# Optimization experiments

Measured on AMD Instinct MI355X. Metric: run time of the kernel, lower is better.

Reference implementation:

```python
import jax, jax.numpy as jnp
import numpy as np

IN_CHANNELS = 512
NUM_HEADS = 8
HEAD_CH = IN_CHANNELS // NUM_HEADS


def setup_inputs() -> dict:
    key = jax.random.key(0)
    k0, k1, k2, k3, k4 = jax.random.split(key, 5)
    B, C, H, W = 4, IN_CHANNELS, 128, 128
    x = jax.random.normal(k0, (B, C, H, W), dtype=jnp.float32)
    # 1x1 Conv2d weights == per-pixel linear layers over channels
    s_in = 1.0 / np.sqrt(C)
    Wqkv = jax.random.uniform(k1, (3 * C, C), dtype=jnp.float32, minval=-s_in, maxval=s_in)
    bqkv = jax.random.uniform(k2, (3 * C,), dtype=jnp.float32, minval=-s_in, maxval=s_in)
    Wout = jax.random.uniform(k3, (C, C), dtype=jnp.float32, minval=-s_in, maxval=s_in)
    bout = jax.random.uniform(k4, (C,), dtype=jnp.float32, minval=-s_in, maxval=s_in)
    return {"x": x, "Wqkv": Wqkv, "bqkv": bqkv, "Wout": Wout, "bout": bout}


def _axial_attention(x, Wqkv, bqkv, Wout, bout):
    B, C, H, W = x.shape
    nh, d = NUM_HEADS, HEAD_CH
    scale = 1.0 / jnp.sqrt(jnp.asarray(d, dtype=x.dtype))

    # 1x1 conv qkv projection: [B, 3C, H, W]
    qkv = jnp.einsum('bchw,oc->bohw', x, Wqkv) + bqkv[None, :, None, None]
    q, k, v = jnp.split(qkv, 3, axis=1)
    # [B, nh, d, H, W]
    q = q.reshape(B, nh, d, H, W)
    k = k.reshape(B, nh, d, H, W)
    v = v.reshape(B, nh, d, H, W)

    # Row attention: for each row h, attend across width (w over u)
    scores_row = jnp.einsum('bndhw,bndhu->bnhwu', q, k) * scale  # [B,nh,H,W,W]
    probs_row = jax.nn.softmax(scores_row, axis=-1)
    out_row = jnp.einsum('bnhwu,bndhu->bndhw', probs_row, v)  # [B,nh,d,H,W]

    # Column attention: for each column w, attend across height (h over g)
    scores_col = jnp.einsum('bndhw,bndgw->bnwhg', q, k) * scale  # [B,nh,W,H,H]
    probs_col = jax.nn.softmax(scores_col, axis=-1)
    out_col = jnp.einsum('bnwhg,bndgw->bndhw', probs_col, v)  # [B,nh,d,H,W]

    out = (out_row + out_col).reshape(B, C, H, W)
    # 1x1 conv output projection
    return jnp.einsum('bchw,oc->bohw', out, Wout) + bout[None, :, None, None]


def reference(x, Wqkv, bqkv, Wout, bout):
    return _axial_attention(x, Wqkv, bqkv, Wout, bout)
```

## Files before the change

kernel.cpp:

```cpp
#include <hip/hip_runtime.h>

#define DI __device__ __forceinline__

typedef __attribute__((ext_vector_type(4))) float f32x4;
typedef __attribute__((ext_vector_type(8))) short s16x8;
typedef __attribute__((ext_vector_type(4))) short s16x4;
typedef unsigned short u16;

DI short f2bf(float f) {
  union { float f; unsigned u; } v; v.f = f;
  unsigned r = v.u + 0x7FFFu + ((v.u >> 16) & 1u);
  return (short)(r >> 16);
}
DI float bf2f(short h) {
  union { unsigned u; float f; } v; v.u = ((unsigned)(u16)h) << 16; return v.f;
}

#define MFMA(a, b, c) __builtin_amdgcn_mfma_f32_16x16x32_bf16((a), (b), (c), 0, 0, 0)

__global__ void cast_weights_kernel(const float* __restrict__ wqkv, u16* __restrict__ wqkv_bf,
                                    const float* __restrict__ wout, u16* __restrict__ wout_bf) {
  const int n1 = 1536 * 512 / 4, n2 = 512 * 512 / 4;
  for (int c = blockIdx.x * blockDim.x + threadIdx.x; c < n1 + n2; c += gridDim.x * blockDim.x) {
    const float4* src; u16* dst; int idx;
    if (c < n1) { src = (const float4*)wqkv; dst = wqkv_bf; idx = c; }
    else        { src = (const float4*)wout; dst = wout_bf; idx = c - n1; }
    float4 v = src[idx];
    s16x4 o;
    o[0] = f2bf(v.x); o[1] = f2bf(v.y); o[2] = f2bf(v.z); o[3] = f2bf(v.w);
    *(s16x4*)(dst + (long)idx * 4) = o;
  }
}

template<bool IN_F32>
__global__ __launch_bounds__(256)
void transpose_kernel(const void* __restrict__ in, u16* __restrict__ out,
                      int in_rstride, int out_rstride, long plane_in, long plane_out) {
  __shared__ __align__(16) u16 t[64][72];
  const int tid = threadIdx.x;
  const long bi = (long)blockIdx.z * plane_in;
  const long bo = (long)blockIdx.z * plane_out;
  const int r0 = blockIdx.y * 64, c0 = blockIdx.x * 64;
#pragma unroll
  for (int i = 0; i < 4; ++i) {
    int c = tid + i * 256;
    int row = c >> 4, c4 = c & 15;
    s16x4 pk;
    if (IN_F32) {
      const float4 v = *(const float4*)((const float*)in + bi + (long)(r0 + row) * in_rstride + c0 + c4 * 4);
      pk[0] = f2bf(v.x); pk[1] = f2bf(v.y); pk[2] = f2bf(v.z); pk[3] = f2bf(v.w);
    } else {
      pk = *(const s16x4*)((const u16*)in + bi + (long)(r0 + row) * in_rstride + c0 + c4 * 4);
    }
    *(s16x4*)&t[row][c4 * 4] = pk;
  }
  __syncthreads();
#pragma unroll
  for (int i = 0; i < 2; ++i) {
    int c = tid + i * 256;
    int orow = c >> 3, u = c & 7;
    s16x8 pk;
#pragma unroll
    for (int j = 0; j < 8; ++j) pk[j] = (short)t[u * 8 + j][orow];
    *(s16x8*)(out + bo + (long)(c0 + orow) * out_rstride + r0 + u * 8) = pk;
  }
}

template<int EPI>
__global__ __launch_bounds__(256, 2)
void gemm_kernel(const u16* __restrict__ A, const u16* __restrict__ B,
                 const float* __restrict__ bias,
                 u16* __restrict__ out_qk, u16* __restrict__ out_v,
                 float* __restrict__ out_f, long b_batch_off, long o_batch_off) {
  __shared__ __align__(16) u16 As[128 * 64];
  __shared__ __align__(16) u16 Bs[128 * 64];
  const int tid = threadIdx.x;
  const int lane = tid & 63, wid = tid >> 6;
  const int l15 = lane & 15, g4 = lane >> 4;
  const int wr = wid >> 1, wc = wid & 1;
  const int m0 = blockIdx.y * 128, n0 = blockIdx.x * 128;
  const u16* Bp = B + (long)blockIdx.z * b_batch_off;

  f32x4 acc[4][4];
#pragma unroll
  for (int i = 0; i < 4; ++i)
#pragma unroll
    for (int j = 0; j < 4; ++j) { f32x4 z = {0.f, 0.f, 0.f, 0.f}; acc[i][j] = z; }

  int rowA[4], uA[4];
#pragma unroll
  for (int i = 0; i < 4; ++i) { int c = tid + i * 256; rowA[i] = c >> 3; uA[i] = c & 7; }

  s16x8 ra[4], rb[4];
  auto gload = [&](int kt) {
#pragma unroll
    for (int i = 0; i < 4; ++i)
      ra[i] = *(const s16x8*)(A + (long)(m0 + rowA[i]) * 512 + kt * 64 + uA[i] * 8);
#pragma unroll
    for (int i = 0; i < 4; ++i)
      rb[i] = *(const s16x8*)(Bp + (long)(n0 + rowA[i]) * 512 + kt * 64 + uA[i] * 8);
  };
  auto sstore = [&]() {
#pragma unroll
    for (int i = 0; i < 4; ++i)
      *(s16x8*)(As + rowA[i] * 64 + ((uA[i] ^ (rowA[i] & 7)) * 8)) = ra[i];
#pragma unroll
    for (int i = 0; i < 4; ++i)
      *(s16x8*)(Bs + rowA[i] * 64 + ((uA[i] ^ (rowA[i] & 7)) * 8)) = rb[i];
  };

  gload(0);
  for (int kt = 0; kt < 8; ++kt) {
    __syncthreads();
    sstore();
    __syncthreads();
    if (kt < 7) gload(kt + 1);
#pragma unroll
    for (int ks = 0; ks < 2; ++ks) {
      s16x8 af[4], bfr[4];
#pragma unroll
      for (int mi = 0; mi < 4; ++mi) {
        int row = (wr * 4 + mi) * 16 + l15;
        af[mi] = *(const s16x8*)(As + row * 64 + (((ks * 4 + g4) ^ (row & 7)) * 8));
      }
#pragma unroll
      for (int ni = 0; ni < 4; ++ni) {
        int row = (wc * 4 + ni) * 16 + l15;
        bfr[ni] = *(const s16x8*)(Bs + row * 64 + (((ks * 4 + g4) ^ (row & 7)) * 8));
      }
#pragma unroll
      for (int mi = 0; mi < 4; ++mi)
#pragma unroll
        for (int ni = 0; ni < 4; ++ni)
          acc[mi][ni] = MFMA(af[mi], bfr[ni], acc[mi][ni]);
    }
  }

  if (EPI == 0) {
    if (m0 < 1024) {
#pragma unroll
      for (int mi = 0; mi < 4; ++mi) {
        int o0 = m0 + (wr * 4 + mi) * 16 + 4 * g4;
        float b0 = bias[o0], b1 = bias[o0 + 1], b2 = bias[o0 + 2], b3 = bias[o0 + 3];
#pragma unroll
        for (int ni = 0; ni < 4; ++ni) {
          int p = n0 + (wc * 4 + ni) * 16 + l15;
          s16x4 pk;
          pk[0] = f2bf(acc[mi][ni][0] + b0);
          pk[1] = f2bf(acc[mi][ni][1] + b1);
          pk[2] = f2bf(acc[mi][ni][2] + b2);
          pk[3] = f2bf(acc[mi][ni][3] + b3);
          *(s16x4*)(out_qk + (long)p * 1024 + o0) = pk;
        }
      }
    } else {
#pragma unroll
      for (int mi = 0; mi < 4; ++mi) {
        int o0 = m0 + (wr * 4 + mi) * 16 + 4 * g4;
#pragma unroll
        for (int ni = 0; ni < 4; ++ni) {
          int p = n0 + (wc * 4 + ni) * 16 + l15;
#pragma unroll
          for (int r = 0; r < 4; ++r)
            out_v[(long)(o0 - 1024 + r) * 16384 + p] = (u16)f2bf(acc[mi][ni][r] + bias[o0 + r]);
        }
      }
    }
  } else {
    float* of = out_f + (long)blockIdx.z * o_batch_off;
#pragma unroll
    for (int mi = 0; mi < 4; ++mi) {
      int o0 = m0 + (wr * 4 + mi) * 16 + 4 * g4;
#pragma unroll
      for (int ni = 0; ni < 4; ++ni) {
        int p = n0 + (wc * 4 + ni) * 16 + l15;
#pragma unroll
        for (int r = 0; r < 4; ++r)
          of[(long)(o0 + r) * 16384 + p] = acc[mi][ni][r] + bias[o0 + r];
      }
    }
  }
}

template<int MODE>
__global__ __launch_bounds__(512, 2)
void attn_kernel(const u16* __restrict__ qk_t, const u16* __restrict__ vsrc,
                 u16* __restrict__ outp) {
  __shared__ __align__(16) u16 smem[24576];
  u16* qT = smem;
  u16* kT = smem + 8192;
  u16* vS = smem + 16384;
  u16* P  = smem;

  const int tid = threadIdx.x;
  const int lane = tid & 63, wid = tid >> 6;
  const int l15 = lane & 15, g4 = lane >> 4;
  const int gidx = blockIdx.x;
  const int n = gidx >> 7, pos = gidx & 127;

  long q_base, q_rstride;
  if (MODE == 0) { q_base = (long)pos * 128 * 1024 + n * 64; q_rstride = 1024; }
  else           { q_base = (long)pos * 1024 + n * 64;       q_rstride = 128 * 1024; }
  const long v_base = (long)n * 64 * 16384 + (long)pos * 128;

#pragma unroll
  for (int i = 0; i < 4; ++i) {
    int c = tid + i * 512;
    int which = c >> 10;
    int cc = c & 1023;
    int row = cc >> 3, u = cc & 7;
    s16x8 val = *(const s16x8*)(qk_t + q_base + which * 512 + (long)row * q_rstride + u * 8);
    u16* dst = which ? kT : qT;
    *(s16x8*)(dst + row * 64 + ((u ^ (row & 7)) * 8)) = val;
  }
#pragma unroll
  for (int i = 0; i < 2; ++i) {
    int c = tid + i * 512;
    int row = c >> 4, u = c & 15;
    s16x8 val = *(const s16x8*)(vsrc + v_base + (long)row * 16384 + u * 8);
    *(s16x8*)(vS + row * 128 + ((u ^ (row & 15)) * 8)) = val;
  }
  __syncthreads();

  f32x4 acc[8];
#pragma unroll
  for (int nt = 0; nt < 8; ++nt) { f32x4 z = {0.f, 0.f, 0.f, 0.f}; acc[nt] = z; }
  s16x8 aq[2];
  {
    int row = wid * 16 + l15;
#pragma unroll
    for (int ks = 0; ks < 2; ++ks)
      aq[ks] = *(const s16x8*)(qT + row * 64 + (((ks * 4 + g4) ^ (row & 7)) * 8));
  }
#pragma unroll
  for (int nt = 0; nt < 8; ++nt) {
    int rowk = nt * 16 + l15;
#pragma unroll
    for (int ks = 0; ks < 2; ++ks) {
      s16x8 bk = *(const s16x8*)(kT + rowk * 64 + (((ks * 4 + g4) ^ (rowk & 7)) * 8));
      acc[nt] = MFMA(aq[ks], bk, acc[nt]);
    }
  }

#pragma unroll
  for (int r = 0; r < 4; ++r) {
    float m = -1e30f;
#pragma unroll
    for (int nt = 0; nt < 8; ++nt) m = fmaxf(m, acc[nt][r]);
    m = fmaxf(m, __shfl_xor(m, 1));
    m = fmaxf(m, __shfl_xor(m, 2));
    m = fmaxf(m, __shfl_xor(m, 4));
    m = fmaxf(m, __shfl_xor(m, 8));
    float s = 0.f;
#pragma unroll
    for (int nt = 0; nt < 8; ++nt) {
      float e = __expf((acc[nt][r] - m) * 0.125f);
      acc[nt][r] = e; s += e;
    }
    s += __shfl_xor(s, 1); s += __shfl_xor(s, 2);
    s += __shfl_xor(s, 4); s += __shfl_xor(s, 8);
    float rinv = 1.0f / s;
#pragma unroll
    for (int nt = 0; nt < 8; ++nt) acc[nt][r] *= rinv;
  }
  __syncthreads();

#pragma unroll
  for (int nt = 0; nt < 8; ++nt) {
    int u = nt * 16 + l15;
#pragma unroll
    for (int r = 0; r < 4; ++r) {
      int w = wid * 16 + 4 * g4 + r;
      int ch = (u >> 3) ^ (w & 15);
      P[w * 128 + ch * 8 + (u & 7)] = (u16)f2bf(acc[nt][r]);
    }
  }
  __syncthreads();

  const int mw = wid >> 2, nw = wid & 3;
  f32x4 pacc[2][2];
#pragma unroll
  for (int mi = 0; mi < 2; ++mi)
#pragma unroll
    for (int ni = 0; ni < 2; ++ni) { f32x4 z = {0.f, 0.f, 0.f, 0.f}; pacc[mi][ni] = z; }
#pragma unroll
  for (int ks = 0; ks < 4; ++ks) {
    s16x8 av[2], bp[2];
#pragma unroll
    for (int mi = 0; mi < 2; ++mi) {
      int d = (mw * 2 + mi) * 16 + l15;
      av[mi] = *(const s16x8*)(vS + d * 128 + (((ks * 4 + g4) ^ (d & 15)) * 8));
    }
#pragma unroll
    for (int ni = 0; ni < 2; ++ni) {
      int w = (nw * 2 + ni) * 16 + l15;
      bp[ni] = *(const s16x8*)(P + w * 128 + (((ks * 4 + g4) ^ (w & 15)) * 8));
    }
#pragma unroll
    for (int mi = 0; mi < 2; ++mi)
#pragma unroll
      for (int ni = 0; ni < 2; ++ni)
        pacc[mi][ni] = MFMA(av[mi], bp[ni], pacc[mi][ni]);
  }

  long out_pbase, out_pstr;
  if (MODE == 0) { out_pbase = (long)pos * 128 * 512; out_pstr = 512; }
  else           { out_pbase = (long)pos * 512;       out_pstr = 128 * 512; }
#pragma unroll
  for (int mi = 0; mi < 2; ++mi) {
    int d0 = (mw * 2 + mi) * 16 + 4 * g4;
#pragma unroll
    for (int ni = 0; ni < 2; ++ni) {
      int nj = (nw * 2 + ni) * 16 + l15;
      long base = out_pbase + (long)nj * out_pstr + n * 64 + d0;
      if (MODE == 0) {
        s16x4 pk;
#pragma unroll
        for (int r = 0; r < 4; ++r) pk[r] = f2bf(pacc[mi][ni][r]);
        *(s16x4*)(outp + base) = pk;
      } else {
        s16x4 old = *(const s16x4*)(outp + base);
        s16x4 pk;
#pragma unroll
        for (int r = 0; r < 4; ++r) pk[r] = f2bf(bf2f(old[r]) + pacc[mi][ni][r]);
        *(s16x4*)(outp + base) = pk;
      }
    }
  }
}

extern "C" void kernel_launch(void* const* d_in, const int* in_sizes, int n_in,
                              void* d_out, int out_size, void* d_ws, size_t ws_size,
                              hipStream_t stream) {
  const float* x    = (const float*)d_in[0];
  const float* wqkv = (const float*)d_in[1];
  const float* bqkv = (const float*)d_in[2];
  const float* wout = (const float*)d_in[3];
  const float* bout = (const float*)d_in[4];
  float* out = (float*)d_out;

  char* ws = (char*)d_ws;
  size_t off = 0;
  auto alloc = [&](size_t bytes) { void* p = ws + off; off += (bytes + 255) & ~(size_t)255; return p; };
  u16* wqkv_bf = (u16*)alloc(1536L * 512 * 2);
  u16* wout_bf = (u16*)alloc(512L * 512 * 2);
  u16* qk_t    = (u16*)alloc(16384L * 1024 * 2);
  u16* v_buf   = (u16*)alloc(512L * 16384 * 2);
  u16* vT      = (u16*)alloc(512L * 16384 * 2);
  u16* xT      = (u16*)alloc(16384L * 512 * 2);
  u16* attn_T  = (u16*)alloc(4L * 16384 * 512 * 2);

  cast_weights_kernel<<<256, 256, 0, stream>>>(wqkv, wqkv_bf, wout, wout_bf);

  for (int b = 0; b < 4; ++b) {
    const float* xb = x + (long)b * 512 * 16384;
    u16* attn_b = attn_T + (long)b * 16384 * 512;
    transpose_kernel<true><<<dim3(256, 8, 1), 256, 0, stream>>>(xb, xT, 16384, 512, 0, 0);
    gemm_kernel<0><<<dim3(128, 12, 1), 256, 0, stream>>>(wqkv_bf, xT, bqkv, qk_t, v_buf,
                                                         nullptr, 0, 0);
    transpose_kernel<false><<<dim3(2, 2, 512), 256, 0, stream>>>(v_buf, vT, 128, 128, 16384, 16384);
    attn_kernel<0><<<dim3(1024), 512, 0, stream>>>(qk_t, v_buf, attn_b);
    attn_kernel<1><<<dim3(1024), 512, 0, stream>>>(qk_t, vT, attn_b);
  }
  gemm_kernel<1><<<dim3(128, 4, 4), 256, 0, stream>>>(wout_bf, attn_T, bout, nullptr, nullptr,
                                                      out, 16384L * 512, 512L * 16384);
}
```

Baseline: 440.7 us.

## Batch all images per launch and stage tiles via direct global-to-LDS loads

Removes the per-batch host loop so every kernel launches once over all four images, with per-batch workspace buffers sized 4x. GEMM and attention staging now use global_load_lds to copy tiles straight into shared memory with the swizzle applied on the source address, instead of going through registers. This drops the register prefetch double-buffering in the GEMM, so the global loads for the next tile no longer overlap with the MFMAs. Larger grids should give better occupancy, at the cost of more workspace memory.

After: 391.1 us. 11.3% less time.

```diff
diff --git a/kernel.cpp b/kernel.cpp
--- a/kernel.cpp
+++ b/kernel.cpp
@@ -6,6 +6,9 @@
 typedef __attribute__((ext_vector_type(8))) short s16x8;
 typedef __attribute__((ext_vector_type(4))) short s16x4;
 typedef unsigned short u16;
+
+#define AS_G(p) ((const __attribute__((address_space(1))) void*)(p))
+#define AS_L(p) ((__attribute__((address_space(3))) void*)(p))
 
 DI short f2bf(float f) {
   union { float f; unsigned u; } v; v.f = f;
@@ -71,7 +74,7 @@
 void gemm_kernel(const u16* __restrict__ A, const u16* __restrict__ B,
                  const float* __restrict__ bias,
                  u16* __restrict__ out_qk, u16* __restrict__ out_v,
-                 float* __restrict__ out_f, long b_batch_off, long o_batch_off) {
+                 float* __restrict__ out_f) {
   __shared__ __align__(16) u16 As[128 * 64];
   __shared__ __align__(16) u16 Bs[128 * 64];
   const int tid = threadIdx.x;
@@ -79,42 +82,38 @@
   const int l15 = lane & 15, g4 = lane >> 4;
   const int wr = wid >> 1, wc = wid & 1;
   const int m0 = blockIdx.y * 128, n0 = blockIdx.x * 128;
-  const u16* Bp = B + (long)blockIdx.z * b_batch_off;
+  const int z = blockIdx.z;
+  const u16* Bp = B + (long)z * 8388608;
 
   f32x4 acc[4][4];
 #pragma unroll
   for (int i = 0; i < 4; ++i)
 #pragma unroll
-    for (int j = 0; j < 4; ++j) { f32x4 z = {0.f, 0.f, 0.f, 0.f}; acc[i][j] = z; }
-
-  int rowA[4], uA[4];
-#pragma unroll
-  for (int i = 0; i < 4; ++i) { int c = tid + i * 256; rowA[i] = c >> 3; uA[i] = c & 7; }
-
-  s16x8 ra[4], rb[4];
-  auto gload = [&](int kt) {
-#pragma unroll
-    for (int i = 0; i < 4; ++i)
-      ra[i] = *(const s16x8*)(A + (long)(m0 + rowA[i]) * 512 + kt * 64 + uA[i] * 8);
-#pragma unroll
-    for (int i = 0; i < 4; ++i)
-      rb[i] = *(const s16x8*)(Bp + (long)(n0 + rowA[i]) * 512 + kt * 64 + uA[i] * 8);
+    for (int j = 0; j < 4; ++j) { f32x4 z4 = {0.f, 0.f, 0.f, 0.f}; acc[i][j] = z4; }
+
+  const int srow = wid * 32 + (lane >> 3);
+  const int su = lane & 7;
+  auto stage = [&](int kt) {
+#pragma unroll
+    for (int i = 0; i < 4; ++i) {
+      int row = srow + i * 8;
+      int ksw = (su ^ (row & 7)) * 8;
+      __builtin_amdgcn_global_load_lds(AS_G(A + (long)(m0 + row) * 512 + kt * 64 + ksw),
+                                       AS_L(As + wid * 2048 + i * 512), 16, 0, 0);
+    }
+#pragma unroll
+    for (int i = 0; i < 4; ++i) {
+      int row = srow + i * 8;
+      int ksw = (su ^ (row & 7)) * 8;
+      __builtin_amdgcn_global_load_lds(AS_G(Bp + (long)(n0 + row) * 512 + kt * 64 + ksw),
+                                       AS_L(Bs + wid * 2048 + i * 512), 16, 0, 0);
+    }
   };
-  auto sstore = [&]() {
-#pragma unroll
-    for (int i = 0; i < 4; ++i)
-      *(s16x8*)(As + rowA[i] * 64 + ((uA[i] ^ (rowA[i] & 7)) * 8)) = ra[i];
-#pragma unroll
-    for (int i = 0; i < 4; ++i)
-      *(s16x8*)(Bs + rowA[i] * 64 + ((uA[i] ^ (rowA[i] & 7)) * 8)) = rb[i];
-  };
-
-  gload(0);
+
   for (int kt = 0; kt < 8; ++kt) {
     __syncthreads();
-    sstore();
+    stage(kt);
     __syncthreads();
-    if (kt < 7) gload(kt + 1);
 #pragma unroll
     for (int ks = 0; ks < 2; ++ks) {
       s16x8 af[4], bfr[4];
@@ -137,6 +136,8 @@
   }
 
   if (EPI == 0) {
+    u16* qk_b = out_qk + (long)z * 16777216;
+    u16* v_b  = out_v + (long)z * 8388608;
     if (m0 < 1024) {
 #pragma unroll
       for (int mi = 0; mi < 4; ++mi) {
@@ -150,7 +151,7 @@
           pk[1] = f2bf(acc[mi][ni][1] + b1);
           pk[2] = f2bf(acc[mi][ni][2] + b2);
           pk[3] = f2bf(acc[mi][ni][3] + b3);
-          *(s16x4*)(out_qk + (long)p * 1024 + o0) = pk;
+          *(s16x4*)(qk_b + (long)p * 1024 + o0) = pk;
         }
       }
     } else {
@@ -162,12 +163,12 @@
           int p = n0 + (wc * 4 + ni) * 16 + l15;
 #pragma unroll
           for (int r = 0; r < 4; ++r)
-            out_v[(long)(o0 - 1024 + r) * 16384 + p] = (u16)f2bf(acc[mi][ni][r] + bias[o0 + r]);
+            v_b[(long)(o0 - 1024 + r) * 16384 + p] = (u16)f2bf(acc[mi][ni][r] + bias[o0 + r]);
         }
       }
     }
   } else {
-    float* of = out_f + (long)blockIdx.z * o_batch_off;
+    float* of = out_f + (long)z * 8388608;
 #pragma unroll
     for (int mi = 0; mi < 4; ++mi) {
       int o0 = m0 + (wr * 4 + mi) * 16 + 4 * g4;
@@ -184,8 +185,8 @@
 
 template<int MODE>
 __global__ __launch_bounds__(512, 2)
-void attn_kernel(const u16* __restrict__ qk_t, const u16* __restrict__ vsrc,
-                 u16* __restrict__ outp) {
+void attn_kernel(const u16* __restrict__ qk_t_g, const u16* __restrict__ vsrc_g,
+                 u16* __restrict__ outp_g) {
   __shared__ __align__(16) u16 smem[24576];
   u16* qT = smem;
   u16* kT = smem + 8192;
@@ -195,8 +196,13 @@
   const int tid = threadIdx.x;
   const int lane = tid & 63, wid = tid >> 6;
   const int l15 = lane & 15, g4 = lane >> 4;
-  const int gidx = blockIdx.x;
+  const int b = blockIdx.x >> 10;
+  const int gidx = blockIdx.x & 1023;
   const int n = gidx >> 7, pos = gidx & 127;
+
+  const u16* qk_t = qk_t_g + (long)b * 16777216;
+  const u16* vsrc = vsrc_g + (long)b * 8388608;
+  u16* outp = outp_g + (long)b * 8388608;
 
   long q_base, q_rstride;
   if (MODE == 0) { q_base = (long)pos * 128 * 1024 + n * 64; q_rstride = 1024; }
@@ -204,21 +210,22 @@
   const long v_base = (long)n * 64 * 16384 + (long)pos * 128;
 
 #pragma unroll
-  for (int i = 0; i < 4; ++i) {
-    int c = tid + i * 512;
-    int which = c >> 10;
-    int cc = c & 1023;
-    int row = cc >> 3, u = cc & 7;
-    s16x8 val = *(const s16x8*)(qk_t + q_base + which * 512 + (long)row * q_rstride + u * 8);
-    u16* dst = which ? kT : qT;
-    *(s16x8*)(dst + row * 64 + ((u ^ (row & 7)) * 8)) = val;
-  }
-#pragma unroll
-  for (int i = 0; i < 2; ++i) {
-    int c = tid + i * 512;
-    int row = c >> 4, u = c & 15;
-    s16x8 val = *(const s16x8*)(vsrc + v_base + (long)row * 16384 + u * 8);
-    *(s16x8*)(vS + row * 128 + ((u ^ (row & 15)) * 8)) = val;
+  for (int j = 0; j < 6; ++j) {
+    int t = wid + j * 8;
+    if (t < 32) {
+      int which = t >> 4;
+      int tt = t & 15;
+      int row = tt * 8 + (lane >> 3);
+      int u = lane & 7;
+      const u16* src = qk_t + q_base + which * 512 + (long)row * q_rstride + ((u ^ (row & 7)) * 8);
+      __builtin_amdgcn_global_load_lds(AS_G(src), AS_L(smem + t * 512), 16, 0, 0);
+    } else {
+      int tt = t - 32;
+      int row = tt * 4 + (lane >> 4);
+      int u = lane & 15;
+      const u16* src = vsrc + v_base + (long)row * 16384 + ((u ^ (row & 15)) * 8);
+      __builtin_amdgcn_global_load_lds(AS_G(src), AS_L(smem + t * 512), 16, 0, 0);
+    }
   }
   __syncthreads();
 
@@ -344,24 +351,18 @@
   auto alloc = [&](size_t bytes) { void* p = ws + off; off += (bytes + 255) & ~(size_t)255; return p; };
   u16* wqkv_bf = (u16*)alloc(1536L * 512 * 2);
   u16* wout_bf = (u16*)alloc(512L * 512 * 2);
-  u16* qk_t    = (u16*)alloc(16384L * 1024 * 2);
-  u16* v_buf   = (u16*)alloc(512L * 16384 * 2);
-  u16* vT      = (u16*)alloc(512L * 16384 * 2);
-  u16* xT      = (u16*)alloc(16384L * 512 * 2);
+  u16* xT      = (u16*)alloc(4L * 16384 * 512 * 2);
+  u16* qk_t    = (u16*)alloc(4L * 16384 * 1024 * 2);
+  u16* v_buf   = (u16*)alloc(4L * 512 * 16384 * 2);
+  u16* vT      = (u16*)alloc(4L * 512 * 16384 * 2);
   u16* attn_T  = (u16*)alloc(4L * 16384 * 512 * 2);
 
   cast_weights_kernel<<<256, 256, 0, stream>>>(wqkv, wqkv_bf, wout, wout_bf);
-
-  for (int b = 0; b < 4; ++b) {
-    const float* xb = x + (long)b * 512 * 16384;
-    u16* attn_b = attn_T + (long)b * 16384 * 512;
-    transpose_kernel<true><<<dim3(256, 8, 1), 256, 0, stream>>>(xb, xT, 16384, 512, 0, 0);
-    gemm_kernel<0><<<dim3(128, 12, 1), 256, 0, stream>>>(wqkv_bf, xT, bqkv, qk_t, v_buf,
-                                                         nullptr, 0, 0);
-    transpose_kernel<false><<<dim3(2, 2, 512), 256, 0, stream>>>(v_buf, vT, 128, 128, 16384, 16384);
-    attn_kernel<0><<<dim3(1024), 512, 0, stream>>>(qk_t, v_buf, attn_b);
-    attn_kernel<1><<<dim3(1024), 512, 0, stream>>>(qk_t, vT, attn_b);
-  }
-  gemm_kernel<1><<<dim3(128, 4, 4), 256, 0, stream>>>(wout_bf, attn_T, bout, nullptr, nullptr,
-                                                      out, 16384L * 512, 512L * 16384);
-}
+  transpose_kernel<true><<<dim3(256, 8, 4), 256, 0, stream>>>(
+      x, xT, 16384, 512, 512L * 16384, 16384L * 512);
+  gemm_kernel<0><<<dim3(128, 12, 4), 256, 0, stream>>>(wqkv_bf, xT, bqkv, qk_t, v_buf, nullptr);
+  transpose_kernel<false><<<dim3(2, 2, 2048), 256, 0, stream>>>(v_buf, vT, 128, 128, 16384, 16384);
+  attn_kernel<0><<<dim3(4096), 512, 0, stream>>>(qk_t, v_buf, attn_T);
+  attn_kernel<1><<<dim3(4096), 512, 0, stream>>>(qk_t, vT, attn_T);
+  gemm_kernel<1><<<dim3(128, 4, 4), 256, 0, stream>>>(wout_bf, attn_T, bout, nullptr, nullptr, out);
+}
```
